# Performance work log

Hardware: AMD Instinct MI355X
Metric: run time of the kernel (lower is better)

## Reference

```python
import jax, jax.numpy as jnp
import numpy as np

EPS = 1e-7
LN_EPS = 1e-6


def project(x):
    norm = jnp.maximum(jnp.linalg.norm(x, axis=-1, keepdims=True), EPS)
    max_norm = 1.0 - EPS
    return jnp.where(norm >= 1.0, x / norm * max_norm, x)


def mobius_add(x, y, c):
    x2 = jnp.sum(x * x, -1, keepdims=True)
    y2 = jnp.sum(y * y, -1, keepdims=True)
    xy = jnp.sum(x * y, -1, keepdims=True)
    num = (1 + 2 * c * xy + c * y2) * x + (1 - c * x2) * y
    den = 1 + 2 * c * xy + c * c * x2 * y2
    return project(num / jnp.maximum(den, EPS))


def logmap0(y, c):
    sqrt_c = jnp.maximum(jnp.sqrt(c), EPS)
    y_norm = jnp.linalg.norm(y, axis=-1, keepdims=True)
    safe = jnp.maximum(y_norm, EPS)
    mag = jnp.arctanh(jnp.minimum(y_norm, 1.0 - EPS)) / sqrt_c
    return jnp.where(y_norm < EPS, jnp.zeros_like(y), mag * (y / safe))


def expmap0(v, c):
    sqrt_c = jnp.maximum(jnp.sqrt(c), EPS)
    v_norm = jnp.linalg.norm(v, axis=-1, keepdims=True)
    safe = jnp.maximum(v_norm, EPS)
    mag = jnp.tanh(sqrt_c * safe) / sqrt_c
    return project(jnp.where(v_norm < EPS, jnp.zeros_like(v), mag * (v / safe)))


def poincare_dist(x, y, c):
    # x: [B,H,N,1,D], y: [B,H,N,W,D], c: [B,1,1,1,1] -> dist [B,H,N,W]
    sqrt_c = jnp.maximum(jnp.sqrt(c), EPS)
    add_norm = jnp.linalg.norm(mobius_add(-x, y, c), axis=-1)
    arg = jnp.minimum(sqrt_c.squeeze(-1) * add_norm, 1.0 - EPS)
    return 2.0 * jnp.arctanh(arg) / sqrt_c.squeeze(-1)


def sliding_windows(x, window):
    # x: [B,H,N,Dh] -> [B,H,N,window,Dh] of the last `window` keys per query (zero-padded)
    B, H, N, Dh = x.shape
    pad = jnp.zeros((B, H, window - 1, Dh), dtype=x.dtype)
    xp = jnp.concatenate([pad, x], axis=2)
    idx = jnp.arange(window)[None, :] + jnp.arange(N)[:, None]  # [N, W]
    return xp[:, :, idx, :]


def layer_norm(x, scale, bias):
    mu = jnp.mean(x, axis=-1, keepdims=True)
    var = jnp.mean(jnp.square(x - mu), axis=-1, keepdims=True)
    return (x - mu) * jax.lax.rsqrt(var + LN_EPS) * scale + bias


def setup_inputs() -> dict:
    key = jax.random.key(0)
    B, N, DIM, H = 2, 1024, 1024, 16
    Dh = DIM // H
    ks = jax.random.split(key, 16)
    s = 1.0 / np.sqrt(DIM)
    x = 0.01 * jax.random.normal(ks[0], (B, N, DIM), jnp.float32)  # well inside the ball
    # rotary angles: pos * inv_freq, shape [N, Dh//2]
    inv_freq = 1.0 / (10000.0 ** (np.arange(0, Dh // 2, dtype=np.float32) * 2.0 / Dh))
    freqs = jnp.asarray(np.arange(N, dtype=np.float32)[:, None] * inv_freq[None, :])
    c = 0.5 + 0.5 * jax.random.uniform(ks[1], (B,), jnp.float32)
    p = {
        'Wq': s * jax.random.normal(ks[2], (DIM, DIM), jnp.float32), 'bq': jnp.zeros((DIM,), jnp.float32),
        'Wk': s * jax.random.normal(ks[3], (DIM, DIM), jnp.float32), 'bk': jnp.zeros((DIM,), jnp.float32),
        'Wv': s * jax.random.normal(ks[4], (DIM, DIM), jnp.float32), 'bv': jnp.zeros((DIM,), jnp.float32),
        'Wo': s * jax.random.normal(ks[5], (DIM, DIM), jnp.float32), 'bo': jnp.zeros((DIM,), jnp.float32),
        'W1': s * jax.random.normal(ks[6], (DIM, 4 * DIM), jnp.float32), 'b1': jnp.zeros((4 * DIM,), jnp.float32),
        'W2': (1.0 / np.sqrt(4 * DIM)) * jax.random.normal(ks[7], (4 * DIM, DIM), jnp.float32), 'b2': jnp.zeros((DIM,), jnp.float32),
        'ln1_scale': jnp.ones((DIM,), jnp.float32), 'ln1_bias': jnp.zeros((DIM,), jnp.float32),
        'ln2_scale': jnp.ones((DIM,), jnp.float32), 'ln2_bias': jnp.zeros((DIM,), jnp.float32),
        'geo_scale': jnp.ones((H, 1, 1), jnp.float32),
    }
    return dict(x=x, freqs=freqs, c=c, **p)


def reference(x, freqs, c, Wq, bq, Wk, bk, Wv, bv, Wo, bo, W1, b1, W2, b2,
              ln1_scale, ln1_bias, ln2_scale, ln2_bias, geo_scale):
    WINDOW = 32
    B, N, DIM = x.shape
    H = geo_scale.shape[0]
    Dh = DIM // H
    c_ln = c.reshape(B, 1, 1)
    c_attn = c.reshape(B, 1, 1, 1)
    c_d = c.reshape(B, 1, 1, 1, 1)

    # tangent-space layer norm 1
    x_norm = expmap0(layer_norm(logmap0(x, c_ln), ln1_scale, ln1_bias), c_ln)
    x_tan = logmap0(x_norm, c_ln)

    q = (x_tan @ Wq + bq).reshape(B, N, H, Dh)
    k = (x_tan @ Wk + bk).reshape(B, N, H, Dh)
    v = (x_tan @ Wv + bv).reshape(B, N, H, Dh)

    # rotary embedding (real-arithmetic form of complex multiply)
    cos = jnp.cos(freqs).reshape(1, N, 1, Dh // 2)
    sin = jnp.sin(freqs).reshape(1, N, 1, Dh // 2)

    def rope(t):
        t_r, t_i = jnp.split(t, 2, -1)
        return jnp.concatenate([t_r * cos - t_i * sin, t_r * sin + t_i * cos], -1)

    q_hyp = expmap0(rope(q), c_attn)
    k_hyp = expmap0(rope(k), c_attn)

    q_t = q_hyp.transpose(0, 2, 1, 3)  # [B,H,N,Dh]
    k_t = k_hyp.transpose(0, 2, 1, 3)
    v_t = v.transpose(0, 2, 1, 3)

    k_w = sliding_windows(k_t, WINDOW)  # [B,H,N,W,Dh]
    v_w = sliding_windows(v_t, WINDOW)

    dist = poincare_dist(q_t[:, :, :, None, :], k_w, c_d)  # [B,H,N,W]
    attn = jax.nn.softmax(-geo_scale * dist, axis=-1)
    attn_out = jnp.einsum('bhnw,bhnwd->bhnd', attn, v_w).transpose(0, 2, 1, 3).reshape(B, N, DIM)

    attn_hyp = expmap0(attn_out @ Wo + bo, c_ln)
    x_att = mobius_add(x, attn_hyp, c_ln)

    # tangent-space layer norm 2 + hyperbolic FFN
    x_norm2 = expmap0(layer_norm(logmap0(x_att, c_ln), ln2_scale, ln2_bias), c_ln)
    t = logmap0(x_norm2, c_ln)
    ffn_tan = jax.nn.gelu(t @ W1 + b1) @ W2 + b2
    x_ffn = expmap0(ffn_tan, c_ln)
    return mobius_add(x_att, x_ffn, c_ln)
```

## Files before the change

kernel.cpp:

```cpp
#include <hip/hip_runtime.h>
#include <cmath>

static constexpr int SEQ = 1024;
static constexpr int DIM = 1024;
static constexpr int NH  = 16;
static constexpr int DH  = 64;
static constexpr int WB  = 2;
static constexpr int ROWS = WB * SEQ;
__device__ static constexpr double D_EPS = 1e-7;

typedef unsigned short ushort_t;
typedef __attribute__((ext_vector_type(8))) short short8v;
typedef __attribute__((ext_vector_type(4))) float float4v;

#define GLOAD_LDS(gp, lp)                                                   \
  __builtin_amdgcn_global_load_lds(                                         \
      (const __attribute__((address_space(1))) uint32_t*)(gp),              \
      (__attribute__((address_space(3))) uint32_t*)(lp), 16, 0, 0)

__device__ __forceinline__ uint32_t bf16_hi_bits(float f) {
  uint32_t u = __float_as_uint(f);
  return (u + 0x7fffu + ((u >> 16) & 1u)) >> 16;
}

__device__ __forceinline__ size_t tiled_addr(int row, int col, int Kld) {
  return ((size_t)(row >> 7) * (Kld >> 5) + (col >> 5)) * 4096
       + (size_t)((((row >> 4) & 7) << 9) + (((col >> 3) & 3) << 7) + ((row & 15) << 3) + (col & 7));
}
__device__ __forceinline__ void store_hl(ushort_t* __restrict__ hi, ushort_t* __restrict__ lo,
                                         size_t addr, float f) {
  const uint32_t hb = bf16_hi_bits(f);
  hi[addr] = (ushort_t)hb;
  lo[addr] = (ushort_t)bf16_hi_bits(f - __uint_as_float(hb << 16));
}

__device__ __forceinline__ double wsum64(double v) {
#pragma unroll
  for (int m = 32; m >= 1; m >>= 1) v += __shfl_xor(v, m, 64);
  return v;
}

__device__ __forceinline__ void conv_w_body(
    const float* __restrict__ W, ushort_t* __restrict__ hi, ushort_t* __restrict__ lo,
    int K, int N, int tid) {
  const int n = tid % N;
  const int k0 = (tid / N) << 3;
  uint32_t hw[4], lw[4];
#pragma unroll
  for (int rp = 0; rp < 4; rp++) {
    uint32_t h2[2], l2[2];
#pragma unroll
    for (int e = 0; e < 2; e++) {
      const float f = W[(size_t)(k0 + rp * 2 + e) * N + n];
      const uint32_t hb = bf16_hi_bits(f);
      h2[e] = hb;
      l2[e] = bf16_hi_bits(f - __uint_as_float(hb << 16));
    }
    hw[rp] = h2[0] | (h2[1] << 16);
    lw[rp] = l2[0] | (l2[1] << 16);
  }
  const size_t addr = tiled_addr(n, k0, K);
  *(uint4*)&hi[addr] = *(uint4*)hw;
  *(uint4*)&lo[addr] = *(uint4*)lw;
}

__global__ __launch_bounds__(256) void conv_all_kernel(
    const float* __restrict__ Wq, const float* __restrict__ Wk,
    const float* __restrict__ Wv, const float* __restrict__ Wo,
    const float* __restrict__ W1,
    ushort_t* __restrict__ qkvo_hi, ushort_t* __restrict__ qkvo_lo,
    ushort_t* __restrict__ w1_hi, ushort_t* __restrict__ w1_lo) {
  const int blk = blockIdx.x;
  if (blk < 2048) {
    const int which = blk >> 9;
    const float* W = (which == 0) ? Wq : (which == 1) ? Wk : (which == 2) ? Wv : Wo;
    const size_t off = (size_t)which << 20;
    conv_w_body(W, qkvo_hi + off, qkvo_lo + off, DIM, DIM,
                (blk & 511) * 256 + threadIdx.x);
  } else {
    conv_w_body(W1, w1_hi, w1_lo, DIM, 4 * DIM, (blk - 2048) * 256 + threadIdx.x);
  }
}

__global__ __launch_bounds__(256) void conv_w_kernel(
    const float* __restrict__ W, ushort_t* __restrict__ hi, ushort_t* __restrict__ lo,
    int K, int N) {
  conv_w_body(W, hi, lo, K, N, blockIdx.x * 256 + threadIdx.x);
}

__device__ __forceinline__ void ln_chain_body(
    const float xv[4], int row, double cc,
    const float* __restrict__ gamma, const float* __restrict__ beta,
    ushort_t* __restrict__ ohi, ushort_t* __restrict__ olo,
    double sh[3][4], int t) {
  double s0 = 0.0, s1 = 0.0;
#pragma unroll
  for (int i = 0; i < 4; i++) {
    s0 += (double)xv[i];
    s1 += (double)xv[i] * (double)xv[i];
  }
  s0 = wsum64(s0); s1 = wsum64(s1);
  const int wid = t >> 6, lane = t & 63;
  __syncthreads();
  if (lane == 0) { sh[0][wid] = s0; sh[1][wid] = s1; }
  __syncthreads();
  s0 = sh[0][0] + sh[0][1] + sh[0][2] + sh[0][3];
  s1 = sh[1][0] + sh[1][1] + sh[1][2] + sh[1][3];

  const double sqc = fmax(sqrt(cc), D_EPS);
  const double xn  = sqrt(s1);
  double a = 0.0;
  if (xn >= D_EPS) a = atanh(fmin(xn, 1.0 - D_EPS)) / sqc / fmax(xn, D_EPS);
  const double mu   = a * s0 / (double)DIM;
  const double var  = a * a * s1 / (double)DIM - mu * mu;
  const double invs = 1.0 / sqrt(var + 1e-6);

  double tv[4]; double s2 = 0.0;
#pragma unroll
  for (int i = 0; i < 4; i++) {
    const int col = t + 256 * i;
    tv[i] = (a * (double)xv[i] - mu) * invs * (double)gamma[col] + (double)beta[col];
    s2 += tv[i] * tv[i];
  }
  s2 = wsum64(s2);
  __syncthreads();
  if (lane == 0) sh[0][wid] = s2;
  __syncthreads();
  s2 = sh[0][0] + sh[0][1] + sh[0][2] + sh[0][3];

  const double tn = sqrt(s2);
  double C = 0.0;
  if (tn >= D_EPS) {
    const double safe_t = fmax(tn, D_EPS);
    const double mag2 = tanh(sqc * safe_t) / sqc;
    const double en = mag2 * (tn / safe_t);
    const double pn = fmax(en, D_EPS);
    const double f  = (pn >= 1.0) ? (1.0 - D_EPS) / pn : 1.0;
    const double yn = en * f;
    if (yn >= D_EPS) {
      const double mag3 = atanh(fmin(yn, 1.0 - D_EPS)) / sqc;
      C = (mag2 / safe_t) * f * (mag3 / fmax(yn, D_EPS));
    }
  }
#pragma unroll
  for (int i = 0; i < 4; i++) {
    const int col = t + 256 * i;
    store_hl(ohi, olo, tiled_addr(row, col, DIM), (float)(tv[i] * C));
  }
}

__global__ __launch_bounds__(256) void ln_tan_kernel(
    const float* __restrict__ xin, const float* __restrict__ cb,
    const float* __restrict__ gamma, const float* __restrict__ beta,
    ushort_t* __restrict__ ohi, ushort_t* __restrict__ olo) {
  __shared__ double sh[3][4];
  const int row = blockIdx.x;
  const int b = row / SEQ;
  const float* xr = xin + (size_t)row * DIM;
  const int t = threadIdx.x;
  float xv[4];
#pragma unroll
  for (int i = 0; i < 4; i++) xv[i] = xr[t + 256 * i];
  ln_chain_body(xv, row, (double)cb[b], gamma, beta, ohi, olo, sh, t);
}

__device__ __forceinline__ void mobius_coef(
    double sx2, double st2, double sxt, double cc, double& Pd, double& Qd) {
  const double sqc = fmax(sqrt(cc), D_EPS);
  const double tn = sqrt(st2);
  double s = 0.0;
  if (tn >= D_EPS) {
    const double safe = fmax(tn, D_EPS);
    const double mag = tanh(sqc * safe) / sqc;
    const double en = mag * (tn / safe);
    const double pn = fmax(en, D_EPS);
    const double f  = (pn >= 1.0) ? (1.0 - D_EPS) / pn : 1.0;
    s = (mag / safe) * f;
  }
  const double x2 = sx2, y2 = s * s * st2, xy = s * sxt;
  const double P   = 1.0 + 2.0 * cc * xy + cc * y2;
  const double Q   = 1.0 - cc * x2;
  const double den = fmax(1.0 + 2.0 * cc * xy + cc * cc * x2 * y2, D_EPS);
  const double num2 = P * P * x2 + Q * Q * y2 + 2.0 * P * Q * xy;
  const double rn  = sqrt(fmax(num2, 0.0)) / den;
  const double pn2 = fmax(rn, D_EPS);
  const double pf  = (pn2 >= 1.0) ? (1.0 - D_EPS) / pn2 : 1.0;
  Pd = (P / den) * pf;
  Qd = (Q / den) * pf * s;
}

__global__ __launch_bounds__(256) void expmobius_parts4_kernel(
    const float* __restrict__ xb,
    const float* __restrict__ p0, const float* __restrict__ p1,
    const float* __restrict__ p2, const float* __restrict__ p3,
    const float* __restrict__ bias, const float* __restrict__ cb,
    float* __restrict__ out) {
  __shared__ double sh[3][4];
  const int row = blockIdx.x;
  const int b = row / SEQ;
  const size_t ro = (size_t)row * DIM;
  const int t = threadIdx.x;
  float xv[4];
  double tv[4];
  double sx2 = 0.0, st2 = 0.0, sxt = 0.0;
#pragma unroll
  for (int i = 0; i < 4; i++) {
    const int col = t + 256 * i;
    xv[i] = xb[ro + col];
    tv[i] = (double)p0[ro + col] + (double)p1[ro + col] +
            (double)p2[ro + col] + (double)p3[ro + col] + (double)bias[col];
    sx2 += (double)xv[i] * (double)xv[i];
    st2 += tv[i] * tv[i];
    sxt += (double)xv[i] * tv[i];
  }
  sx2 = wsum64(sx2); st2 = wsum64(st2); sxt = wsum64(sxt);
  const int wid = t >> 6, lane = t & 63;
  if (lane == 0) { sh[0][wid] = sx2; sh[1][wid] = st2; sh[2][wid] = sxt; }
  __syncthreads();
  sx2 = sh[0][0] + sh[0][1] + sh[0][2] + sh[0][3];
  st2 = sh[1][0] + sh[1][1] + sh[1][2] + sh[1][3];
  sxt = sh[2][0] + sh[2][1] + sh[2][2] + sh[2][3];
  double Pd, Qd;
  mobius_coef(sx2, st2, sxt, (double)cb[b], Pd, Qd);
#pragma unroll
  for (int i = 0; i < 4; i++)
    out[ro + t + 256 * i] = (float)(Pd * (double)xv[i] + Qd * tv[i]);
}

__global__ __launch_bounds__(256) void expmobius_ln_kernel(
    const float* __restrict__ xb,
    const float* __restrict__ p0, const float* __restrict__ p1,
    const float* __restrict__ p2, const float* __restrict__ p3,
    const float* __restrict__ bias, const float* __restrict__ cb,
    const float* __restrict__ gamma, const float* __restrict__ beta,
    float* __restrict__ out, ushort_t* __restrict__ ohi, ushort_t* __restrict__ olo) {
  __shared__ double sh[3][4];
  const int row = blockIdx.x;
  const int b = row / SEQ;
  const size_t ro = (size_t)row * DIM;
  const int t = threadIdx.x;
  float xv[4];
  double tv[4];
  double sx2 = 0.0, st2 = 0.0, sxt = 0.0;
#pragma unroll
  for (int i = 0; i < 4; i++) {
    const int col = t + 256 * i;
    xv[i] = xb[ro + col];
    tv[i] = (double)p0[ro + col] + (double)p1[ro + col] +
            (double)p2[ro + col] + (double)p3[ro + col] + (double)bias[col];
    sx2 += (double)xv[i] * (double)xv[i];
    st2 += tv[i] * tv[i];
    sxt += (double)xv[i] * tv[i];
  }
  sx2 = wsum64(sx2); st2 = wsum64(st2); sxt = wsum64(sxt);
  const int wid = t >> 6, lane = t & 63;
  if (lane == 0) { sh[0][wid] = sx2; sh[1][wid] = st2; sh[2][wid] = sxt; }
  __syncthreads();
  sx2 = sh[0][0] + sh[0][1] + sh[0][2] + sh[0][3];
  st2 = sh[1][0] + sh[1][1] + sh[1][2] + sh[1][3];
  sxt = sh[2][0] + sh[2][1] + sh[2][2] + sh[2][3];
  const double cc = (double)cb[b];
  double Pd, Qd;
  mobius_coef(sx2, st2, sxt, cc, Pd, Qd);
  float ov[4];
#pragma unroll
  for (int i = 0; i < 4; i++) {
    ov[i] = (float)(Pd * (double)xv[i] + Qd * tv[i]);
    out[ro + t + 256 * i] = ov[i];
  }
  ln_chain_body(ov, row, cc, gamma, beta, ohi, olo, sh, t);
}

__global__ __launch_bounds__(256) void rope_expmap_kernel(
    float* __restrict__ q, float* __restrict__ k,
    const float* __restrict__ freqs, const float* __restrict__ cb) {
  const int row = blockIdx.x;
  const int b = row / SEQ, n = row % SEQ;
  const int t = threadIdx.x;
  const int h = t >> 4, j = t & 15;
  const int p1 = j, p2 = j + 16;
  const double f1 = (double)freqs[n * (DH / 2) + p1];
  const double f2 = (double)freqs[n * (DH / 2) + p2];
  const double c1 = cos(f1), s1 = sin(f1);
  const double c2 = cos(f2), s2 = sin(f2);
  const double cc  = (double)cb[b];
  const double sqc = fmax(sqrt(cc), D_EPS);
  const size_t base = (size_t)row * DIM + (size_t)h * DH;
  float* arrs[2] = {q, k};
#pragma unroll
  for (int a = 0; a < 2; a++) {
    float* p = arrs[a] + base;
    const double xr1 = p[p1], xi1 = p[p1 + 32];
    const double xr2 = p[p2], xi2 = p[p2 + 32];
    const double r1 = xr1 * c1 - xi1 * s1, i1 = xr1 * s1 + xi1 * c1;
    const double r2 = xr2 * c2 - xi2 * s2, i2 = xr2 * s2 + xi2 * c2;
    double nrm2 = r1 * r1 + i1 * i1 + r2 * r2 + i2 * i2;
#pragma unroll
    for (int m = 8; m >= 1; m >>= 1) nrm2 += __shfl_xor(nrm2, m, 16);
    const double vn = sqrt(nrm2);
    double sc = 0.0;
    if (vn >= D_EPS) {
      const double safe = fmax(vn, D_EPS);
      const double mag = tanh(sqc * safe) / sqc;
      const double en = mag * (vn / safe);
      const double pn = fmax(en, D_EPS);
      const double f  = (pn >= 1.0) ? (1.0 - D_EPS) / pn : 1.0;
      sc = (mag / safe) * f;
    }
    p[p1] = (float)(r1 * sc); p[p1 + 32] = (float)(i1 * sc);
    p[p2] = (float)(r2 * sc); p[p2 + 32] = (float)(i2 * sc);
  }
}

__global__ __launch_bounds__(256) void attn_kernel(
    const float* __restrict__ qh, const float* __restrict__ kh,
    const float* __restrict__ v, const float* __restrict__ cb,
    const float* __restrict__ geo,
    ushort_t* __restrict__ ohi, ushort_t* __restrict__ olo) {
  __shared__ float qs[8][DH];
  const int g = threadIdx.x >> 5;
  const int w = threadIdx.x & 31;
  const int gid = blockIdx.x * 8 + g;
  const int n = gid & (SEQ - 1);
  const int bh = gid >> 10;
  const int h = bh & (NH - 1);
  const int b = bh >> 4;
  const int row = b * SEQ + n;
  const size_t qbase = (size_t)row * DIM + (size_t)h * DH;
  qs[g][w] = qh[qbase + w];
  qs[g][w + 32] = qh[qbase + w + 32];
  __syncthreads();

  const double cc  = (double)cb[b];
  const double sqc = fmax(sqrt(cc), D_EPS);
  double q2p = (double)qs[g][w] * qs[g][w] + (double)qs[g][w + 32] * qs[g][w + 32];
#pragma unroll
  for (int m = 16; m >= 1; m >>= 1) q2p += __shfl_xor(q2p, m, 32);
  const double a2 = q2p;

  const int msrc = n - 31 + w;
  double y2 = 0.0, qy = 0.0;
  if (msrc >= 0) {
    const float* kr = kh + ((size_t)(b * SEQ + msrc)) * DIM + (size_t)h * DH;
#pragma unroll 8
    for (int d = 0; d < DH; d++) {
      const double kv = (double)kr[d];
      y2 += kv * kv;
      qy += (double)qs[g][d] * kv;
    }
  }
  const double ay = -qy;
  const double P = 1.0 + 2.0 * cc * ay + cc * y2;
  const double Q = 1.0 - cc * a2;
  const double den = fmax(1.0 + 2.0 * cc * ay + cc * cc * a2 * y2, D_EPS);
  const double num2 = P * P * a2 + Q * Q * y2 + 2.0 * P * Q * ay;
  const double rn = sqrt(fmax(num2, 0.0)) / den;
  const double pn = fmax(rn, D_EPS);
  const double addn = (pn >= 1.0) ? (1.0 - D_EPS) * (rn / pn) : rn;
  const double arg = fmin(sqc * addn, 1.0 - D_EPS);
  const double dist = 2.0 * atanh(arg) / sqc;
  const double logit = -(double)geo[h] * dist;

  double mx = logit;
#pragma unroll
  for (int m = 16; m >= 1; m >>= 1) mx = fmax(mx, __shfl_xor(mx, m, 32));
  const double e = exp(logit - mx);
  double se = e;
#pragma unroll
  for (int m = 16; m >= 1; m >>= 1) se += __shfl_xor(se, m, 32);
  const double p = e / se;

  double acc1 = 0.0, acc2 = 0.0;
  for (int wp = 0; wp < 32; wp++) {
    const double pw = __shfl(p, wp, 32);
    const int mp = n - 31 + wp;
    if (mp >= 0) {
      const float* vr = v + ((size_t)(b * SEQ + mp)) * DIM + (size_t)h * DH;
      acc1 += pw * (double)vr[w];
      acc2 += pw * (double)vr[w + 32];
    }
  }
  const int col = h * DH + w;
  store_hl(ohi, olo, tiled_addr(row, col, DIM), (float)acc1);
  store_hl(ohi, olo, tiled_addr(row, col + 32, DIM), (float)acc2);
}

__device__ __forceinline__ float gelu_tanh(float x) {
  const float x3 = x * x * x;
  return 0.5f * x * (1.0f + tanhf(0.7978845608028654f * (x + 0.044715f * x3)));
}

template <int EPI>
__device__ __forceinline__ void mfma_gemm_body(
    const ushort_t* __restrict__ Ahi, const ushort_t* __restrict__ Alo, int Kld,
    const ushort_t* __restrict__ Bhi, const ushort_t* __restrict__ Blo, int KB,
    const float* __restrict__ bias, float* __restrict__ Cf,
    ushort_t* __restrict__ Chi, ushort_t* __restrict__ Clo, int KldOut,
    int N, int k0, int klen, int m0, int n0) {
  __shared__ __align__(16) ushort_t AsH[4096], AsL[4096], BsH[4096], BsL[4096];
  const int t = threadIdx.x;
  const int lane = t & 63, wave = t >> 6;
  const int wm = (wave >> 1) << 6, wn = (wave & 1) << 6;
  const size_t abase = (size_t)(m0 >> 7) * (Kld >> 5) * 4096;
  const size_t bbase = (size_t)(n0 >> 7) * (KB >> 5) * 4096;

  float4v acc[4][4];
#pragma unroll
  for (int i = 0; i < 4; i++)
#pragma unroll
    for (int j = 0; j < 4; j++) acc[i][j] = (float4v){0.f, 0.f, 0.f, 0.f};

  for (int kt = 0; kt < klen; kt += 32) {
    const size_t at = abase + (size_t)((k0 + kt) >> 5) * 4096;
    const size_t bt = bbase + (size_t)((k0 + kt) >> 5) * 4096;
    __syncthreads();
#pragma unroll
    for (int r = 0; r < 2; r++) {
      const int go = (r << 11) + (t << 3);
      const int lo = (r << 11) + (wave << 9);
      GLOAD_LDS(Ahi + at + go, AsH + lo);
      GLOAD_LDS(Alo + at + go, AsL + lo);
      GLOAD_LDS(Bhi + bt + go, BsH + lo);
      GLOAD_LDS(Blo + bt + go, BsL + lo);
    }
    __syncthreads();
    short8v aH[4], aL[4];
    const int ams = wm >> 4;
#pragma unroll
    for (int im = 0; im < 4; im++) {
      const int off = ((((ams + im) << 6) + lane) << 3);
      aH[im] = *(const short8v*)&AsH[off];
      aL[im] = *(const short8v*)&AsL[off];
    }
    const int bns = wn >> 4;
#pragma unroll
    for (int in_ = 0; in_ < 4; in_++) {
      const int off = ((((bns + in_) << 6) + lane) << 3);
      const short8v bH = *(const short8v*)&BsH[off];
      const short8v bL = *(const short8v*)&BsL[off];
#pragma unroll
      for (int im = 0; im < 4; im++) {
        acc[im][in_] = __builtin_amdgcn_mfma_f32_16x16x32_bf16(aH[im], bH, acc[im][in_], 0, 0, 0);
        acc[im][in_] = __builtin_amdgcn_mfma_f32_16x16x32_bf16(aH[im], bL, acc[im][in_], 0, 0, 0);
        acc[im][in_] = __builtin_amdgcn_mfma_f32_16x16x32_bf16(aL[im], bH, acc[im][in_], 0, 0, 0);
      }
    }
  }
  const int cq = lane >> 4, ci = lane & 15;
#pragma unroll
  for (int im = 0; im < 4; im++) {
    const int row = m0 + wm + im * 16 + cq * 4;
#pragma unroll
    for (int in_ = 0; in_ < 4; in_++) {
      const int col = n0 + wn + in_ * 16 + ci;
      if (EPI == 2) {
#pragma unroll
        for (int r = 0; r < 4; r++) Cf[(size_t)(row + r) * N + col] = acc[im][in_][r];
      } else if (EPI == 0) {
        const float bv_ = bias[col];
#pragma unroll
        for (int r = 0; r < 4; r++) Cf[(size_t)(row + r) * N + col] = acc[im][in_][r] + bv_;
      } else {
        const float bv_ = bias[col];
#pragma unroll
        for (int r = 0; r < 4; r++)
          store_hl(Chi, Clo, tiled_addr(row + r, col, KldOut),
                   gelu_tanh(acc[im][in_][r] + bv_));
      }
    }
  }
}

__global__ __launch_bounds__(256) void qkv_mfma(
    const ushort_t* __restrict__ Ahi, const ushort_t* __restrict__ Alo,
    const ushort_t* __restrict__ Whi, const ushort_t* __restrict__ Wlo,
    const float* __restrict__ bq, const float* __restrict__ bk, const float* __restrict__ bv,
    float* __restrict__ Cq, float* __restrict__ Ck, float* __restrict__ Cv) {
  const int which = blockIdx.x >> 3;
  const int n0 = (blockIdx.x & 7) << 7;
  const size_t woff = (size_t)which << 20;
  const float* bias = (which == 0) ? bq : (which == 1) ? bk : bv;
  float* C = (which == 0) ? Cq : (which == 1) ? Ck : Cv;
  mfma_gemm_body<0>(Ahi, Alo, DIM, Whi + woff, Wlo + woff, DIM, bias, C,
                    nullptr, nullptr, 0, DIM, 0, DIM, blockIdx.y << 7, n0);
}

__global__ __launch_bounds__(256) void ffn_up_mfma(
    const ushort_t* __restrict__ Ahi, const ushort_t* __restrict__ Alo,
    const ushort_t* __restrict__ W1hi, const ushort_t* __restrict__ W1lo,
    const float* __restrict__ b1, ushort_t* __restrict__ Hhi, ushort_t* __restrict__ Hlo) {
  mfma_gemm_body<1>(Ahi, Alo, DIM, W1hi, W1lo, DIM, b1, nullptr, Hhi, Hlo, 4 * DIM,
                    4 * DIM, 0, DIM, blockIdx.y << 7, blockIdx.x << 7);
}

__global__ __launch_bounds__(256) void gemm_splitk_mfma(
    const ushort_t* __restrict__ Ahi, const ushort_t* __restrict__ Alo, int Kld,
    const ushort_t* __restrict__ Bhi, const ushort_t* __restrict__ Blo, int KB,
    float* __restrict__ C0, float* __restrict__ C1,
    float* __restrict__ C2, float* __restrict__ C3, int N, int klen) {
  const int z = blockIdx.z;
  float* C = (z == 0) ? C0 : (z == 1) ? C1 : (z == 2) ? C2 : C3;
  mfma_gemm_body<2>(Ahi, Alo, Kld, Bhi, Blo, KB, nullptr, C, nullptr, nullptr, 0,
                    N, z * klen, klen, blockIdx.y << 7, blockIdx.x << 7);
}

extern "C" void kernel_launch(void* const* d_in, const int* in_sizes, int n_in,
                              void* d_out, int out_size, void* d_ws, size_t ws_size,
                              hipStream_t stream) {
  const float* x     = (const float*)d_in[0];
  const float* freqs = (const float*)d_in[1];
  const float* c     = (const float*)d_in[2];
  const float* Wq = (const float*)d_in[3];  const float* bq = (const float*)d_in[4];
  const float* Wk = (const float*)d_in[5];  const float* bk = (const float*)d_in[6];
  const float* Wv = (const float*)d_in[7];  const float* bv = (const float*)d_in[8];
  const float* Wo = (const float*)d_in[9];  const float* bo = (const float*)d_in[10];
  const float* W1 = (const float*)d_in[11]; const float* b1 = (const float*)d_in[12];
  const float* W2 = (const float*)d_in[13]; const float* b2 = (const float*)d_in[14];
  const float* g1 = (const float*)d_in[15]; const float* be1 = (const float*)d_in[16];
  const float* g2 = (const float*)d_in[17]; const float* be2 = (const float*)d_in[18];
  const float* geo = (const float*)d_in[19];
  float* out = (float*)d_out;
  float* ws = (float*)d_ws;

  const size_t SZ = (size_t)ROWS * DIM;
  const size_t PL = SZ;
  const uint32_t M1 = 1u << 20;
  auto us = [&](int i) { return (ushort_t*)(ws + (size_t)i * SZ); };

  ushort_t* xt_hi = us(0);           ushort_t* xt_lo = us(0) + PL;
  float* qb = ws + 1 * SZ; float* kb = ws + 2 * SZ; float* vb = ws + 3 * SZ;
  ushort_t* at_hi = us(4);           ushort_t* at_lo = us(4) + PL;
  ushort_t* qkvo_hi = us(5);         ushort_t* qkvo_lo = us(6);
  ushort_t* w1_hi = us(7);           ushort_t* w1_lo = us(8);
  ushort_t* w2_hi = us(5);           ushort_t* w2_lo = us(6);
  ushort_t* t2_hi = us(4);           ushort_t* t2_lo = us(4) + PL;
  ushort_t* h1_hi = us(0);           ushort_t* h1_lo = us(2);
  float* x_att = out;

  conv_all_kernel<<<4096, 256, 0, stream>>>(
      Wq, Wk, Wv, Wo, W1, qkvo_hi, qkvo_lo, w1_hi, w1_lo);
  ln_tan_kernel<<<ROWS, 256, 0, stream>>>(x, c, g1, be1, xt_hi, xt_lo);
  qkv_mfma<<<dim3(24, ROWS / 128), 256, 0, stream>>>(
      xt_hi, xt_lo, qkvo_hi, qkvo_lo, bq, bk, bv, qb, kb, vb);
  rope_expmap_kernel<<<ROWS, 256, 0, stream>>>(qb, kb, freqs, c);
  attn_kernel<<<WB * NH * SEQ / 8, 256, 0, stream>>>(qb, kb, vb, c, geo, at_hi, at_lo);
  gemm_splitk_mfma<<<dim3(DIM / 128, ROWS / 128, 4), 256, 0, stream>>>(
      at_hi, at_lo, DIM, qkvo_hi + 3 * M1, qkvo_lo + 3 * M1, DIM,
      ws + 0 * SZ, ws + 1 * SZ, ws + 2 * SZ, ws + 3 * SZ, DIM, DIM / 4);
  conv_w_kernel<<<2048, 256, 0, stream>>>(W2, w2_hi, w2_lo, 4 * DIM, DIM);
  expmobius_ln_kernel<<<ROWS, 256, 0, stream>>>(
      x, ws + 0 * SZ, ws + 1 * SZ, ws + 2 * SZ, ws + 3 * SZ, bo, c,
      g2, be2, x_att, t2_hi, t2_lo);
  ffn_up_mfma<<<dim3(4 * DIM / 128, ROWS / 128), 256, 0, stream>>>(
      t2_hi, t2_lo, w1_hi, w1_lo, b1, h1_hi, h1_lo);
  gemm_splitk_mfma<<<dim3(DIM / 128, ROWS / 128, 4), 256, 0, stream>>>(
      h1_hi, h1_lo, 4 * DIM, w2_hi, w2_lo, 4 * DIM,
      ws + 4 * SZ, ws + 7 * SZ, ws + 8 * SZ, ws + 9 * SZ, DIM, DIM);
  expmobius_parts4_kernel<<<ROWS, 256, 0, stream>>>(
      x_att, ws + 4 * SZ, ws + 7 * SZ, ws + 8 * SZ, ws + 9 * SZ, b2, c, out);
  (void)in_sizes; (void)n_in; (void)out_size; (void)ws_size;
}
```

Before: 413.8 us.

## Precompute q/k squared norms in rope kernel and vectorize attention loads

The rope/expmap kernel now writes per-head squared norms of the final q and k rows to workspace, so the attention kernel reads them instead of recomputing the q norm reduction and the k norm inside its dot loop. The q·k dot product loads k and q as float4, and the V accumulation loads float2 with each lane owning adjacent columns, which changes the output column mapping. This is meant to cut per-lane scalar global loads and double-precision work in the attention kernel, at the cost of a small extra write and extra shuffles in the rope kernel.

```diff
diff --git a/kernel.cpp b/kernel.cpp
--- a/kernel.cpp
+++ b/kernel.cpp
@@ -273,7 +273,8 @@
 
 __global__ __launch_bounds__(256) void rope_expmap_kernel(
     float* __restrict__ q, float* __restrict__ k,
-    const float* __restrict__ freqs, const float* __restrict__ cb) {
+    const float* __restrict__ freqs, const float* __restrict__ cb,
+    double* __restrict__ q2d, double* __restrict__ k2d) {
   const int row = blockIdx.x;
   const int b = row / SEQ, n = row % SEQ;
   const int t = threadIdx.x;
@@ -287,6 +288,7 @@
   const double sqc = fmax(sqrt(cc), D_EPS);
   const size_t base = (size_t)row * DIM + (size_t)h * DH;
   float* arrs[2] = {q, k};
+  double* outs[2] = {q2d, k2d};
 #pragma unroll
   for (int a = 0; a < 2; a++) {
     float* p = arrs[a] + base;
@@ -307,8 +309,14 @@
       const double f  = (pn >= 1.0) ? (1.0 - D_EPS) / pn : 1.0;
       sc = (mag / safe) * f;
     }
-    p[p1] = (float)(r1 * sc); p[p1 + 32] = (float)(i1 * sc);
-    p[p2] = (float)(r2 * sc); p[p2 + 32] = (float)(i2 * sc);
+    const float o1 = (float)(r1 * sc), o2 = (float)(i1 * sc);
+    const float o3 = (float)(r2 * sc), o4 = (float)(i2 * sc);
+    p[p1] = o1; p[p1 + 32] = o2;
+    p[p2] = o3; p[p2 + 32] = o4;
+    double s2 = (double)o1 * o1 + (double)o2 * o2 + (double)o3 * o3 + (double)o4 * o4;
+#pragma unroll
+    for (int m = 8; m >= 1; m >>= 1) s2 += __shfl_xor(s2, m, 16);
+    if (j == 0) outs[a][row * NH + h] = s2;
   }
 }
 
@@ -316,8 +324,9 @@
     const float* __restrict__ qh, const float* __restrict__ kh,
     const float* __restrict__ v, const float* __restrict__ cb,
     const float* __restrict__ geo,
+    const double* __restrict__ q2d, const double* __restrict__ k2d,
     ushort_t* __restrict__ ohi, ushort_t* __restrict__ olo) {
-  __shared__ float qs[8][DH];
+  __shared__ __align__(16) float qs[8][DH];
   const int g = threadIdx.x >> 5;
   const int w = threadIdx.x & 31;
   const int gid = blockIdx.x * 8 + g;
@@ -333,20 +342,23 @@
 
   const double cc  = (double)cb[b];
   const double sqc = fmax(sqrt(cc), D_EPS);
-  double q2p = (double)qs[g][w] * qs[g][w] + (double)qs[g][w + 32] * qs[g][w + 32];
-#pragma unroll
-  for (int m = 16; m >= 1; m >>= 1) q2p += __shfl_xor(q2p, m, 32);
-  const double a2 = q2p;
+  const double a2 = q2d[row * NH + h];
 
   const int msrc = n - 31 + w;
   double y2 = 0.0, qy = 0.0;
   if (msrc >= 0) {
-    const float* kr = kh + ((size_t)(b * SEQ + msrc)) * DIM + (size_t)h * DH;
-#pragma unroll 8
-    for (int d = 0; d < DH; d++) {
-      const double kv = (double)kr[d];
-      y2 += kv * kv;
-      qy += (double)qs[g][d] * kv;
+    const int krow = b * SEQ + msrc;
+    y2 = k2d[krow * NH + h];
+    const float4* kr4 = (const float4*)(kh + (size_t)krow * DIM + (size_t)h * DH);
+    const float4* qs4 = (const float4*)qs[g];
+#pragma unroll
+    for (int d = 0; d < 16; d++) {
+      const float4 kv = kr4[d];
+      const float4 qv = qs4[d];
+      qy += (double)qv.x * (double)kv.x;
+      qy += (double)qv.y * (double)kv.y;
+      qy += (double)qv.z * (double)kv.z;
+      qy += (double)qv.w * (double)kv.w;
     }
   }
   const double ay = -qy;
@@ -375,14 +387,14 @@
     const double pw = __shfl(p, wp, 32);
     const int mp = n - 31 + wp;
     if (mp >= 0) {
-      const float* vr = v + ((size_t)(b * SEQ + mp)) * DIM + (size_t)h * DH;
-      acc1 += pw * (double)vr[w];
-      acc2 += pw * (double)vr[w + 32];
-    }
-  }
-  const int col = h * DH + w;
+      const float2 vv = ((const float2*)(v + ((size_t)(b * SEQ + mp)) * DIM + (size_t)h * DH))[w];
+      acc1 += pw * (double)vv.x;
+      acc2 += pw * (double)vv.y;
+    }
+  }
+  const int col = h * DH + 2 * w;
   store_hl(ohi, olo, tiled_addr(row, col, DIM), (float)acc1);
-  store_hl(ohi, olo, tiled_addr(row, col + 32, DIM), (float)acc2);
+  store_hl(ohi, olo, tiled_addr(row, col + 1, DIM), (float)acc2);
 }
 
 __device__ __forceinline__ float gelu_tanh(float x) {
@@ -535,6 +547,8 @@
   ushort_t* w2_hi = us(5);           ushort_t* w2_lo = us(6);
   ushort_t* t2_hi = us(4);           ushort_t* t2_lo = us(4) + PL;
   ushort_t* h1_hi = us(0);           ushort_t* h1_lo = us(2);
+  double* q2d = (double*)(ws + 9 * SZ);
+  double* k2d = q2d + (size_t)ROWS * NH;
   float* x_att = out;
 
   conv_all_kernel<<<4096, 256, 0, stream>>>(
@@ -542,8 +556,9 @@
   ln_tan_kernel<<<ROWS, 256, 0, stream>>>(x, c, g1, be1, xt_hi, xt_lo);
   qkv_mfma<<<dim3(24, ROWS / 128), 256, 0, stream>>>(
       xt_hi, xt_lo, qkvo_hi, qkvo_lo, bq, bk, bv, qb, kb, vb);
-  rope_expmap_kernel<<<ROWS, 256, 0, stream>>>(qb, kb, freqs, c);
-  attn_kernel<<<WB * NH * SEQ / 8, 256, 0, stream>>>(qb, kb, vb, c, geo, at_hi, at_lo);
+  rope_expmap_kernel<<<ROWS, 256, 0, stream>>>(qb, kb, freqs, c, q2d, k2d);
+  attn_kernel<<<WB * NH * SEQ / 8, 256, 0, stream>>>(
+      qb, kb, vb, c, geo, q2d, k2d, at_hi, at_lo);
   gemm_splitk_mfma<<<dim3(DIM / 128, ROWS / 128, 4), 256, 0, stream>>>(
       at_hi, at_lo, DIM, qkvo_hi + 3 * M1, qkvo_lo + 3 * M1, DIM,
       ws + 0 * SZ, ws + 1 * SZ, ws + 2 * SZ, ws + 3 * SZ, DIM, DIM / 4);
```

Result: slower. 432.4 us (+4.5%).
